# Kernel tuning notes

Hardware: AMD Instinct MI355X
Metric: run time of the kernel (lower is better)

Reference implementation:

```python
import jax, jax.numpy as jnp
import numpy as np

# --- SLAYER hyperparameters (from netParams) ---
THETA = 10.0        # spike threshold
TAU_SR = 10.0       # SRM alpha-kernel time constant (ms)
TAU_RHO = 1.0       # surrogate-gradient width
SCALE_RHO = 1.0     # surrogate-gradient scale
TS = 1.0            # simulation step (ms)
T_SAMPLE = 300      # number of time steps
K_LEN = 64          # truncated SRM kernel length

N_BATCH, N_IN, N_HID, N_OUT = 128, 784, 410, 10


def srm_kernel():
    # SRM-alpha kernel eps(t) = (t/tau) * exp(1 - t/tau), sampled at Ts, eps(0)=0
    t = jnp.arange(K_LEN, dtype=jnp.float32) * TS
    return (t / TAU_SR) * jnp.exp(1.0 - t / TAU_SR)


def psp(x):
    # Causal FIR filtering along time: out[t] = sum_k eps[k] * x[t-k]
    # x: [N, C, T]
    n, c, t = x.shape
    kern = srm_kernel()
    lhs = x.reshape(n * c, 1, t)
    rhs = kern[::-1].reshape(1, 1, K_LEN)  # flip: conv_general_dilated is cross-correlation
    out = jax.lax.conv_general_dilated(
        lhs, rhs, window_strides=(1,), padding=[(K_LEN - 1, 0)],
        dimension_numbers=("NCH", "OIH", "NCH"))
    return out.reshape(n, c, t)


@jax.custom_vjp
def spike_fn(u):
    # Heaviside threshold with surrogate gradient rho(u) = (scale/tau) * exp(-|u-theta|/tau)
    return (u >= THETA).astype(u.dtype)

def _spike_fwd(u):
    return spike_fn(u), u

def _spike_bwd(u, g):
    return (g * (SCALE_RHO / TAU_RHO) * jnp.exp(-jnp.abs(u - THETA) / TAU_RHO),)

spike_fn.defvjp(_spike_fwd, _spike_bwd)


def setup_inputs() -> dict:
    key = jax.random.key(0)
    k1, k2, k3, k4 = jax.random.split(key, 4)
    img = jax.random.uniform(k1, (N_BATCH, N_IN), dtype=jnp.float32)
    rand_u = jax.random.uniform(k2, (N_BATCH, N_IN, T_SAMPLE), dtype=jnp.float32)
    W1 = jax.random.normal(k3, (N_HID, N_IN), dtype=jnp.float32)
    W2 = jax.random.normal(k4, (N_OUT, N_HID), dtype=jnp.float32)
    return {"img": img, "rand_u": rand_u, "W1": W1, "W2": W2}


def reference(img, rand_u, W1, W2):
    # Poisson spike encoding: spike whenever uniform noise < pixel intensity
    s0 = (rand_u < img[:, :, None]).astype(jnp.float32)        # [N, 784, T]
    # fc1 (dense over spatial features, shared over time) -> psp -> spike
    a1 = jnp.einsum("nit,oi->not", s0, W1)                     # [N, 410, T]
    s1 = spike_fn(psp(a1))
    # fc2 -> psp -> spike
    a2 = jnp.einsum("nht,oh->not", s1, W2)                     # [N, 10, T]
    s2 = spike_fn(psp(a2))
    return s2
```

## Files before the change

### kernel.cpp

```cpp
#include <hip/hip_runtime.h>
#include <cstdint>
#include <cstddef>

#define N_B 128
#define N_I 784
#define N_H 410
#define N_O 10
#define TT  300
#define KL  64
#define NK  832
#define NKS 13
#define NTILES 26
#define NDIG 4
#define NKS2 7
#define S1_TILE 4800
#define S1_NSTRIDE 134400
#define SEGL 19
#define SEGL2 10
#define NWG1 (NTILES * N_B)
#define WPX  (NWG1 / 8)
#define DBYTES (NTILES * NKS * 1024)
#define PACKBLK (5 * NKS * N_B)
#define PREPBLK (NDIG * NTILES * NKS + NDIG * NKS2)

typedef int v4i __attribute__((ext_vector_type(4)));

__device__ __forceinline__ void glds16(const void* g, void* l) {
  __builtin_amdgcn_global_load_lds(
      (const __attribute__((address_space(1))) uint32_t*)g,
      (__attribute__((address_space(3))) uint32_t*)l, 16, 0, 0);
}

__global__ void k_prep(const float* __restrict__ rand_u, const float* __restrict__ img,
                       const float* __restrict__ W1, const float* __restrict__ W2,
                       uint8_t* __restrict__ s0b, v4i* __restrict__ Bf,
                       v4i* __restrict__ Bf2) {
  int bid0 = blockIdx.x;
  int lane = threadIdx.x;
  if (bid0 < PACKBLK) {
    int t  = (bid0 % 5) * 64 + lane;
    int w2 = (bid0 / 5) % NKS;
    int n  = bid0 / (5 * NKS);
    if (t >= TT) return;
    const float* rb = rand_u + (size_t)n * N_I * TT + t;
    const float* ib = img + (size_t)n * N_I;
    uint8_t* dst = s0b + ((size_t)n * TT + t) * NK + w2 * 64;
    int kb = w2 * 64;
    #pragma unroll
    for (int g = 0; g < 4; ++g) {
      uint32_t wd[4];
      #pragma unroll
      for (int q = 0; q < 4; ++q) {
        uint32_t v = 0;
        #pragma unroll
        for (int b = 0; b < 4; ++b) {
          int i = kb + g * 16 + q * 4 + b;
          float r = (i < N_I) ? rb[(size_t)i * TT] : 2.0f;
          float p = (i < N_I) ? ib[i] : 0.0f;
          v |= (r < p ? 1u : 0u) << (8 * b);
        }
        wd[q] = v;
      }
      v4i o; o[0] = (int)wd[0]; o[1] = (int)wd[1]; o[2] = (int)wd[2]; o[3] = (int)wd[3];
      *(v4i*)(dst + g * 16) = o;
    }
    return;
  }
  int bid = bid0 - PACKBLK;
  if (bid < NDIG * NTILES * NKS) {
    int ks   = bid % NKS;
    int rest = bid / NKS;
    int nt   = rest % NTILES;
    int d    = rest / NTILES;
    int o     = nt * 16 + (lane & 15);
    int kbase = ks * 64 + (lane >> 4) * 16;
    uint32_t wds[4] = {0, 0, 0, 0};
    for (int j = 0; j < 16; ++j) {
      int k = kbase + j;
      int dig = 0;
      if (o < N_H && k < N_I) {
        double w = (double)W1[(size_t)o * N_I + k];
        int r = (int)llround(w * 268435456.0);
        for (int dd = 0; dd <= d; ++dd) {
          dig = (int)(int8_t)(uint8_t)(r & 255);
          r = (r - dig) >> 8;
        }
      }
      wds[j >> 2] |= ((uint32_t)(uint8_t)(int8_t)dig) << (8 * (j & 3));
    }
    v4i v; v[0] = (int)wds[0]; v[1] = (int)wds[1]; v[2] = (int)wds[2]; v[3] = (int)wds[3];
    Bf[(size_t)bid * 64 + lane] = v;
  } else {
    int b2 = bid - NDIG * NTILES * NKS;
    int ks = b2 % NKS2, d = b2 / NKS2;
    int o     = lane & 15;
    int kbase = ks * 64 + (lane >> 4) * 16;
    uint32_t wds[4] = {0, 0, 0, 0};
    for (int j = 0; j < 16; ++j) {
      int k = kbase + j;
      int dig = 0;
      if (o < N_O && k < N_H) {
        double w = (double)W2[(size_t)o * N_H + k];
        int r = (int)llround(w * 268435456.0);
        for (int dd = 0; dd <= d; ++dd) {
          dig = (int)(int8_t)(uint8_t)(r & 255);
          r = (r - dig) >> 8;
        }
      }
      wds[j >> 2] |= ((uint32_t)(uint8_t)(int8_t)dig) << (8 * (j & 3));
    }
    v4i v; v[0] = (int)wds[0]; v[1] = (int)wds[1]; v[2] = (int)wds[2]; v[3] = (int)wds[3];
    Bf2[(size_t)b2 * 64 + lane] = v;
  }
}

__global__ __launch_bounds__(256) void k_fused2(const uint8_t* __restrict__ s0b,
                                                const v4i* __restrict__ Bf,
                                                uint8_t* __restrict__ s1) {
  __shared__ __align__(16) uint8_t smem[53248];
  uint8_t* bufA = smem;
  uint8_t* bufB = smem + 40960;
  double (*tile)[17] = (double (*)[17])smem;

  int tid = threadIdx.x;
  int wave = tid >> 6, lane = tid & 63;
  int bid = blockIdx.x;
  int sw = (bid & 7) * WPX + (bid >> 3);
  int n = sw / NTILES, nt = sw % NTILES;
  int lrow = lane & 15, quad = lane >> 4;

  const uint8_t* an0 = s0b + (size_t)n * TT * NK;
  int arow = wave * 80 + (lane & 15);
  int acolg = (lane >> 4) * 16;
  const uint8_t* bsrc = (const uint8_t*)Bf + (size_t)nt * NKS * 1024
                      + (size_t)wave * DBYTES + (size_t)lane * 16;

  auto STAGE = [&](int k, int pa, int pb) {
    uint8_t* ad = bufA + pa * 20480 + wave * 5120;
    #pragma unroll
    for (int c = 0; c < 5; ++c) {
      int r = arow + c * 16; if (r > TT - 1) r = TT - 1;
      glds16(an0 + (size_t)r * NK + (size_t)k * 64 + acolg, ad + c * 1024);
    }
    glds16(bsrc + (size_t)k * 1024, bufB + pb * 4096 + wave * 1024);
  };

  v4i acc[5][NDIG];
  #pragma unroll
  for (int m = 0; m < 5; ++m)
    #pragma unroll
    for (int d = 0; d < NDIG; ++d) { acc[m][d][0]=0; acc[m][d][1]=0; acc[m][d][2]=0; acc[m][d][3]=0; }

  STAGE(0, 0, 0);
  STAGE(1, 1, 1);

  #pragma unroll
  for (int ks = 0; ks < NKS; ++ks) {
    if (ks < NKS - 1) { asm volatile("s_waitcnt vmcnt(6)" ::: "memory"); }
    else              { asm volatile("s_waitcnt vmcnt(0)" ::: "memory"); }
    __builtin_amdgcn_s_barrier();
    __builtin_amdgcn_sched_barrier(0);
    v4i a[5], b[NDIG];
    {
      const uint8_t* base = bufA + (ks & 1) * 20480 + wave * 5120 + quad * 256 + lrow * 16;
      #pragma unroll
      for (int m = 0; m < 5; ++m) a[m] = *(const v4i*)(base + m * 1024);
    }
    {
      const uint8_t* base = bufB + (ks % 3) * 4096 + lane * 16;
      #pragma unroll
      for (int d = 0; d < NDIG; ++d) b[d] = *(const v4i*)(base + d * 1024);
    }
    #pragma unroll
    for (int m = 0; m < 5; ++m)
      #pragma unroll
      for (int d = 0; d < NDIG; ++d)
        acc[m][d] = __builtin_amdgcn_mfma_i32_16x16x64_i8(a[m], b[d], acc[m][d], 0, 0, 0);
    asm volatile("s_waitcnt lgkmcnt(0)" ::: "memory");
    __builtin_amdgcn_sched_barrier(0);
    if (ks <= NKS - 3) STAGE(ks + 2, (ks + 2) & 1, (ks + 2) % 3);
  }

  __syncthreads();

  #pragma unroll
  for (int m5 = 0; m5 < 5; ++m5)
    #pragma unroll
    for (int r = 0; r < 4; ++r) {
      int m = wave * 80 + m5 * 16 + quad * 4 + r;
      if (m < TT) {
        double v = (double)acc[m5][0][r]
                 + 256.0      * (double)acc[m5][1][r]
                 + 65536.0    * (double)acc[m5][2][r]
                 + 16777216.0 * (double)acc[m5][3][r];
        tile[m][lrow] = v;
      }
    }
  __syncthreads();

  {
    int col = tid & 15;
    int seg = tid >> 4;
    int T0 = seg * SEGL;
    int Wc = T0 - 63; if (Wc < 0) Wc = 0;
    const double q   = exp(-0.1);
    const double q64 = exp(-6.4);
    const double cS  = (exp(1.0) / 10.0) * (1.0 / 268435456.0);
    double s1a = 0.0, s2a = 0.0, s1b = 0.0, s2b = 0.0;
    uint8_t* sb = s1 + (size_t)n * S1_NSTRIDE + (size_t)nt * S1_TILE + col;
    for (int j = 0; j < 63; ++j) {
      int t = T0 - 63 + j;
      int tc = (t < 0) ? 0 : t;
      double xa = (t >= 0) ? tile[tc][col] : 0.0;
      s2a = q * (s2a + s1a);
      s1a = q * s1a + xa;
    }
    for (int j = 0; j < SEGL; ++j) {
      int t = T0 + j;
      int tc = (t > TT - 1) ? TT - 1 : t;
      int tb = t - 64;
      int tbc = (tb < 0) ? 0 : tb;
      double xa = tile[tc][col];
      double xb = (tb >= Wc) ? tile[tbc][col] : 0.0;
      s2b = q * (s2b + s1b);
      s1b = q * s1b + xb;
      s2a = q * (s2a + s1a);
      s1a = q * s1a + xa;
      double y = cS * (s2a - q64 * (s2b + 64.0 * s1b));
      if (t < TT) sb[(size_t)t * 16] = (y >= 10.0) ? 1 : 0;
    }
  }
}

__global__ __launch_bounds__(256) void k_l2f(const uint8_t* __restrict__ s1,
                                             const v4i* __restrict__ Bf2,
                                             float* __restrict__ out) {
  __shared__ double tile2[TT][17];
  int tid = threadIdx.x;
  int wave = tid >> 6, lane = tid & 63;
  int half = blockIdx.x, n = blockIdx.y;
  int lrow = lane & 15, quad = lane >> 4;
  const uint8_t* s1n = s1 + (size_t)n * S1_NSTRIDE;
  for (int mt = wave; mt < 19; mt += 4) {
    int m0 = mt * 16;
    int trow = m0 + lrow; if (trow > TT - 1) trow = TT - 1;
    v4i acc[NDIG];
    #pragma unroll
    for (int d = 0; d < NDIG; ++d) { acc[d][0]=0; acc[d][1]=0; acc[d][2]=0; acc[d][3]=0; }
    for (int ks = 0; ks < NKS2; ++ks) {
      v4i af = *(const v4i*)(s1n + (size_t)(ks * 4 + quad) * S1_TILE + (size_t)trow * 16);
      #pragma unroll
      for (int d = 0; d < NDIG; ++d) {
        v4i bf = Bf2[(size_t)(d * NKS2 + ks) * 64 + lane];
        acc[d] = __builtin_amdgcn_mfma_i32_16x16x64_i8(af, bf, acc[d], 0, 0, 0);
      }
    }
    #pragma unroll
    for (int r = 0; r < 4; ++r) {
      int m = m0 + quad * 4 + r;
      if (m < TT && lrow < N_O) {
        double v = (double)acc[0][r]
                 + 256.0      * (double)acc[1][r]
                 + 65536.0    * (double)acc[2][r]
                 + 16777216.0 * (double)acc[3][r];
        tile2[m][lrow] = v;
      }
    }
  }
  __syncthreads();

  {
    int col = tid & 15;
    int seg = half * 16 + (tid >> 4);
    int T0 = seg * SEGL2;
    int Wc = T0 - 63; if (Wc < 0) Wc = 0;
    const double q   = exp(-0.1);
    const double q64 = exp(-6.4);
    const double cS  = (exp(1.0) / 10.0) * (1.0 / 268435456.0);
    double s1a = 0.0, s2a = 0.0, s1b = 0.0, s2b = 0.0;
    float* ob = out + (size_t)n * N_O * TT + (size_t)col * TT;
    for (int j = 0; j < 63; ++j) {
      int t = T0 - 63 + j;
      int tc = (t < 0) ? 0 : t;
      tc = (tc > TT - 1) ? TT - 1 : tc;
      double xa = (t >= 0 && t < TT) ? tile2[tc][col] : 0.0;
      s2a = q * (s2a + s1a);
      s1a = q * s1a + xa;
    }
    for (int j = 0; j < SEGL2; ++j) {
      int t = T0 + j;
      int tc = (t > TT - 1) ? TT - 1 : t;
      int tb = t - 64;
      int tbc = (tb < 0) ? 0 : tb;
      tbc = (tbc > TT - 1) ? TT - 1 : tbc;
      double xa = tile2[tc][col];
      double xb = (tb >= Wc) ? tile2[tbc][col] : 0.0;
      s2b = q * (s2b + s1b);
      s1b = q * s1b + xb;
      s2a = q * (s2a + s1a);
      s1a = q * s1a + xa;
      double y = cS * (s2a - q64 * (s2b + 64.0 * s1b));
      if (t < TT && col < N_O) ob[t] = (y >= 10.0) ? 1.0f : 0.0f;
    }
  }
}

extern "C" void kernel_launch(void* const* d_in, const int* in_sizes, int n_in,
                              void* d_out, int out_size, void* d_ws, size_t ws_size,
                              hipStream_t stream) {
  const float* img   = (const float*)d_in[0];
  const float* randu = (const float*)d_in[1];
  const float* W1    = (const float*)d_in[2];
  const float* W2    = (const float*)d_in[3];
  float* out = (float*)d_out;

  char* ws = (char*)d_ws;
  size_t off = 0;
  auto alloc = [&](size_t bytes) -> void* {
    void* p = ws + off;
    off = (off + bytes + 511) & ~(size_t)511;
    return p;
  };
  uint8_t*  s0b = (uint8_t*) alloc((size_t)N_B * TT * NK);
  v4i*      Bf  = (v4i*)     alloc((size_t)NDIG * NTILES * NKS * 64 * 16);
  v4i*      Bf2 = (v4i*)     alloc((size_t)NDIG * NKS2 * 64 * 16);
  uint8_t*  s1  = (uint8_t*) alloc((size_t)N_B * S1_NSTRIDE);
  if (off > ws_size) return;

  k_prep  <<<dim3(PACKBLK + PREPBLK), 64, 0, stream>>>(randu, img, W1, W2, s0b, Bf, Bf2);
  k_fused2<<<dim3(NWG1), 256, 0, stream>>>(s0b, Bf, s1);
  k_l2f   <<<dim3(2, N_B), 256, 0, stream>>>(s1, Bf2, out);
}
```

Measured before the change: 318.8 us.

## Load GEMM operands directly into registers and specialize the PSP scan by segment

Replaces the LDS-staged global_load_lds pipeline in the fused layer-1 kernel with per-lane direct global loads into register buffers (A triple-buffered, B double-buffered), removing block barriers and LDS staging inside the K loop. The PSP recurrence is split so waves past the first skip the boundary clamps and the masking branches. The threshold comparison now uses a prescaled constant in place of a multiply. The risks are higher register pressure and uncoalesced 16-byte row loads from global memory, and the rescaled threshold may round differently from the original comparison.

```diff
diff --git a/kernel.cpp b/kernel.cpp
--- a/kernel.cpp
+++ b/kernel.cpp
@@ -19,17 +19,10 @@
 #define SEGL2 10
 #define NWG1 (NTILES * N_B)
 #define WPX  (NWG1 / 8)
-#define DBYTES (NTILES * NKS * 1024)
 #define PACKBLK (5 * NKS * N_B)
 #define PREPBLK (NDIG * NTILES * NKS + NDIG * NKS2)
 
 typedef int v4i __attribute__((ext_vector_type(4)));
-
-__device__ __forceinline__ void glds16(const void* g, void* l) {
-  __builtin_amdgcn_global_load_lds(
-      (const __attribute__((address_space(1))) uint32_t*)g,
-      (__attribute__((address_space(3))) uint32_t*)l, 16, 0, 0);
-}
 
 __global__ void k_prep(const float* __restrict__ rand_u, const float* __restrict__ img,
                        const float* __restrict__ W1, const float* __restrict__ W2,
@@ -117,11 +110,7 @@
 __global__ __launch_bounds__(256) void k_fused2(const uint8_t* __restrict__ s0b,
                                                 const v4i* __restrict__ Bf,
                                                 uint8_t* __restrict__ s1) {
-  __shared__ __align__(16) uint8_t smem[53248];
-  uint8_t* bufA = smem;
-  uint8_t* bufB = smem + 40960;
-  double (*tile)[17] = (double (*)[17])smem;
-
+  __shared__ double tile[TT][17];
   int tid = threadIdx.x;
   int wave = tid >> 6, lane = tid & 63;
   int bid = blockIdx.x;
@@ -129,21 +118,16 @@
   int n = sw / NTILES, nt = sw % NTILES;
   int lrow = lane & 15, quad = lane >> 4;
 
-  const uint8_t* an0 = s0b + (size_t)n * TT * NK;
-  int arow = wave * 80 + (lane & 15);
-  int acolg = (lane >> 4) * 16;
-  const uint8_t* bsrc = (const uint8_t*)Bf + (size_t)nt * NKS * 1024
-                      + (size_t)wave * DBYTES + (size_t)lane * 16;
-
-  auto STAGE = [&](int k, int pa, int pb) {
-    uint8_t* ad = bufA + pa * 20480 + wave * 5120;
-    #pragma unroll
-    for (int c = 0; c < 5; ++c) {
-      int r = arow + c * 16; if (r > TT - 1) r = TT - 1;
-      glds16(an0 + (size_t)r * NK + (size_t)k * 64 + acolg, ad + c * 1024);
-    }
-    glds16(bsrc + (size_t)k * 1024, bufB + pb * 4096 + wave * 1024);
-  };
+  const v4i* bb = Bf + (size_t)nt * NKS * 64 + lane;
+  const size_t dstr = (size_t)NTILES * NKS * 64;
+  const uint8_t* an = s0b + (size_t)n * TT * NK + quad * 16;
+  const uint8_t* ap[5];
+  #pragma unroll
+  for (int m = 0; m < 5; ++m) {
+    int rr = wave * 80 + m * 16 + lrow;
+    if (rr > TT - 1) rr = TT - 1;
+    ap[m] = an + (size_t)rr * NK;
+  }
 
   v4i acc[5][NDIG];
   #pragma unroll
@@ -151,37 +135,34 @@
     #pragma unroll
     for (int d = 0; d < NDIG; ++d) { acc[m][d][0]=0; acc[m][d][1]=0; acc[m][d][2]=0; acc[m][d][3]=0; }
 
-  STAGE(0, 0, 0);
-  STAGE(1, 1, 1);
+  v4i a[3][5], b[2][4];
+  #pragma unroll
+  for (int m = 0; m < 5; ++m) a[0][m] = *(const v4i*)(ap[m]);
+  #pragma unroll
+  for (int d = 0; d < NDIG; ++d) b[0][d] = bb[(size_t)d * dstr];
+  #pragma unroll
+  for (int m = 0; m < 5; ++m) a[1][m] = *(const v4i*)(ap[m] + 64);
+  #pragma unroll
+  for (int d = 0; d < NDIG; ++d) b[1][d] = bb[(size_t)d * dstr + 64];
 
   #pragma unroll
   for (int ks = 0; ks < NKS; ++ks) {
-    if (ks < NKS - 1) { asm volatile("s_waitcnt vmcnt(6)" ::: "memory"); }
-    else              { asm volatile("s_waitcnt vmcnt(0)" ::: "memory"); }
-    __builtin_amdgcn_s_barrier();
-    __builtin_amdgcn_sched_barrier(0);
-    v4i a[5], b[NDIG];
-    {
-      const uint8_t* base = bufA + (ks & 1) * 20480 + wave * 5120 + quad * 256 + lrow * 16;
-      #pragma unroll
-      for (int m = 0; m < 5; ++m) a[m] = *(const v4i*)(base + m * 1024);
-    }
-    {
-      const uint8_t* base = bufB + (ks % 3) * 4096 + lane * 16;
-      #pragma unroll
-      for (int d = 0; d < NDIG; ++d) b[d] = *(const v4i*)(base + d * 1024);
+    if (ks + 2 < NKS) {
+      #pragma unroll
+      for (int m = 0; m < 5; ++m)
+        a[(ks + 2) % 3][m] = *(const v4i*)(ap[m] + (ks + 2) * 64);
     }
     #pragma unroll
     for (int m = 0; m < 5; ++m)
       #pragma unroll
       for (int d = 0; d < NDIG; ++d)
-        acc[m][d] = __builtin_amdgcn_mfma_i32_16x16x64_i8(a[m], b[d], acc[m][d], 0, 0, 0);
-    asm volatile("s_waitcnt lgkmcnt(0)" ::: "memory");
-    __builtin_amdgcn_sched_barrier(0);
-    if (ks <= NKS - 3) STAGE(ks + 2, (ks + 2) & 1, (ks + 2) % 3);
-  }
-
-  __syncthreads();
+        acc[m][d] = __builtin_amdgcn_mfma_i32_16x16x64_i8(a[ks % 3][m], b[ks & 1][d], acc[m][d], 0, 0, 0);
+    if (ks + 2 < NKS) {
+      #pragma unroll
+      for (int d = 0; d < NDIG; ++d)
+        b[(ks + 2) & 1][d] = bb[(size_t)d * dstr + (ks + 2) * 64];
+    }
+  }
 
   #pragma unroll
   for (int m5 = 0; m5 < 5; ++m5)
@@ -202,32 +183,62 @@
     int col = tid & 15;
     int seg = tid >> 4;
     int T0 = seg * SEGL;
-    int Wc = T0 - 63; if (Wc < 0) Wc = 0;
     const double q   = exp(-0.1);
     const double q64 = exp(-6.4);
     const double cS  = (exp(1.0) / 10.0) * (1.0 / 268435456.0);
+    const double thr = 10.0 / cS;
     double s1a = 0.0, s2a = 0.0, s1b = 0.0, s2b = 0.0;
     uint8_t* sb = s1 + (size_t)n * S1_NSTRIDE + (size_t)nt * S1_TILE + col;
-    for (int j = 0; j < 63; ++j) {
-      int t = T0 - 63 + j;
-      int tc = (t < 0) ? 0 : t;
-      double xa = (t >= 0) ? tile[tc][col] : 0.0;
-      s2a = q * (s2a + s1a);
-      s1a = q * s1a + xa;
-    }
-    for (int j = 0; j < SEGL; ++j) {
-      int t = T0 + j;
-      int tc = (t > TT - 1) ? TT - 1 : t;
-      int tb = t - 64;
-      int tbc = (tb < 0) ? 0 : tb;
-      double xa = tile[tc][col];
-      double xb = (tb >= Wc) ? tile[tbc][col] : 0.0;
-      s2b = q * (s2b + s1b);
-      s1b = q * s1b + xb;
-      s2a = q * (s2a + s1a);
-      s1a = q * s1a + xa;
-      double y = cS * (s2a - q64 * (s2b + 64.0 * s1b));
-      if (t < TT) sb[(size_t)t * 16] = (y >= 10.0) ? 1 : 0;
+    if (wave == 0) {
+      int Wc = T0 - 63; if (Wc < 0) Wc = 0;
+      for (int j = 0; j < 63; ++j) {
+        int t = T0 - 63 + j;
+        int tc = (t < 0) ? 0 : t;
+        double xa = (t >= 0) ? tile[tc][col] : 0.0;
+        s2a = q * (s2a + s1a);
+        s1a = q * s1a + xa;
+      }
+      for (int j = 0; j < SEGL; ++j) {
+        int t = T0 + j;
+        int tc = (t > TT - 1) ? TT - 1 : t;
+        int tb = t - 64;
+        int tbc = (tb < 0) ? 0 : tb;
+        double xa = tile[tc][col];
+        double xb = (tb >= Wc) ? tile[tbc][col] : 0.0;
+        s2b = q * (s2b + s1b);
+        s1b = q * s1b + xb;
+        s2a = q * (s2a + s1a);
+        s1a = q * s1a + xa;
+        double z = s2a - q64 * (s2b + 64.0 * s1b);
+        if (t < TT) sb[(size_t)t * 16] = (z >= thr) ? 1 : 0;
+      }
+    } else {
+      int W0 = T0 - 63;
+      #pragma unroll 7
+      for (int j = 0; j < 63; ++j) {
+        double xa = tile[W0 + j][col];
+        s2a = q * (s2a + s1a);
+        s1a = q * s1a + xa;
+      }
+      {
+        double xa = tile[T0][col];
+        s2a = q * (s2a + s1a);
+        s1a = q * s1a + xa;
+        sb[(size_t)T0 * 16] = (s2a >= thr) ? 1 : 0;
+      }
+      #pragma unroll 6
+      for (int j = 1; j < SEGL; ++j) {
+        int t = T0 + j;
+        int tc = (t > TT - 1) ? TT - 1 : t;
+        double xa = tile[tc][col];
+        double xb = tile[t - 64][col];
+        s2b = q * (s2b + s1b);
+        s1b = q * s1b + xb;
+        s2a = q * (s2a + s1a);
+        s1a = q * s1a + xa;
+        double z = s2a - q64 * (s2b + 64.0 * s1b);
+        if (t < TT) sb[(size_t)t * 16] = (z >= thr) ? 1 : 0;
+      }
     }
   }
 }
@@ -277,6 +288,7 @@
     const double q   = exp(-0.1);
     const double q64 = exp(-6.4);
     const double cS  = (exp(1.0) / 10.0) * (1.0 / 268435456.0);
+    const double thr = 10.0 / cS;
     double s1a = 0.0, s2a = 0.0, s1b = 0.0, s2b = 0.0;
     float* ob = out + (size_t)n * N_O * TT + (size_t)col * TT;
     for (int j = 0; j < 63; ++j) {
@@ -299,8 +311,8 @@
       s1b = q * s1b + xb;
       s2a = q * (s2a + s1a);
       s1a = q * s1a + xa;
-      double y = cS * (s2a - q64 * (s2b + 64.0 * s1b));
-      if (t < TT && col < N_O) ob[t] = (y >= 10.0) ? 1.0f : 0.0f;
+      double z = s2a - q64 * (s2b + 64.0 * s1b);
+      if (t < TT && col < N_O) ob[t] = (z >= thr) ? 1.0f : 0.0f;
     }
   }
 }
```

Result: slower. 339.9 us (+6.6%).
